# Optimization experiments

Measured on AMD Instinct MI355X. Metric: run time of the kernel, lower is better.

## Reference

```python
import jax, jax.numpy as jnp
import numpy as np

N_QUBITS = 8
N_LAYERS = 2
BATCH = 16384


def setup_inputs() -> dict:
    key = jax.random.key(0)
    k1, k2 = jax.random.split(key)
    inputs = jax.random.normal(k1, (BATCH, N_QUBITS), dtype=jnp.float32)
    theta = (jax.random.normal(k2, (N_LAYERS, N_QUBITS, 3), dtype=jnp.float32) * 0.1)
    return {"inputs": inputs, "theta": theta}


def _apply_1q(state, U, q):
    # state: [B, 2, 2, ..., 2] (n qubit axes, wire q -> axis q+1)
    # U: [2, 2] (shared) or [B, 2, 2] (per-sample)
    s = jnp.moveaxis(state, q + 1, -1)
    if U.ndim == 3:
        s = jnp.einsum('bij,b...j->b...i', U, s)
    else:
        s = jnp.einsum('ij,b...j->b...i', U, s)
    return jnp.moveaxis(s, -1, q + 1)


def _cnot(state, c, t):
    # flip target axis where control bit == 1
    s0 = jax.lax.index_in_dim(state, 0, axis=c + 1, keepdims=True)
    s1 = jax.lax.index_in_dim(state, 1, axis=c + 1, keepdims=True)
    s1 = jnp.flip(s1, axis=t + 1)
    return jnp.concatenate([s0, s1], axis=c + 1)


def _circuit(inputs, theta):
    n = N_QUBITS
    B = inputs.shape[0]
    x = jnp.clip(inputs, -1.0, 1.0)
    # |0...0> initial state, batched
    state = jnp.zeros((B, 2 ** n), dtype=jnp.complex64).at[:, 0].set(1.0)
    state = state.reshape((B,) + (2,) * n)

    # ---- angle encoding: RY(pi * x_i) on wire i (per-sample gates) ----
    half = 0.5 * jnp.pi * x  # [B, n]
    c, s = jnp.cos(half), jnp.sin(half)
    for q in range(n):
        U = jnp.stack([jnp.stack([c[:, q], -s[:, q]], -1),
                       jnp.stack([s[:, q], c[:, q]], -1)], -2).astype(jnp.complex64)
        state = _apply_1q(state, U, q)

    # ---- variational layers: Rot(phi,th,om) = RZ(om) RY(th) RZ(phi), then CNOT chain ----
    for layer in range(N_LAYERS):
        for q in range(n):
            phi, th, om = theta[layer, q, 0], theta[layer, q, 1], theta[layer, q, 2]
            ct, st = jnp.cos(0.5 * th), jnp.sin(0.5 * th)
            u00 = jnp.exp(-0.5j * (phi + om)) * ct
            u01 = -jnp.exp(0.5j * (phi - om)) * st
            u10 = jnp.exp(-0.5j * (phi - om)) * st
            u11 = jnp.exp(0.5j * (phi + om)) * ct
            U = jnp.stack([jnp.stack([u00, u01]), jnp.stack([u10, u11])]).astype(jnp.complex64)
            state = _apply_1q(state, U, q)
        for q in range(n - 1):
            state = _cnot(state, q, q + 1)

    # ---- <Z_q> for each wire: marginal prob over qubit q ----
    prob = jnp.real(state * jnp.conj(state))  # [B, 2,...,2]
    exps = []
    for q in range(n):
        axes = tuple(a for a in range(1, n + 1) if a != q + 1)
        m = prob.sum(axis=axes)  # [B, 2]
        exps.append(m[:, 0] - m[:, 1])
    return jnp.stack(exps, axis=-1).astype(jnp.float32)  # [B, n]


def reference(inputs, theta):
    return _circuit(inputs, theta)
```

## Files before the change

### kernel.cpp

```cpp
#include <hip/hip_runtime.h>

#define PI_HALF_F 1.57079632679489661923f

template<int CTRL>
__device__ __forceinline__ float dpp1(float v) {
    return __int_as_float(__builtin_amdgcn_update_dpp(
        0, __float_as_int(v), CTRL, 0xF, 0xF, true));
}
#define QP_XOR1   0xB1
#define QP_XOR2   0x4E
#define QP_XOR3   0x1B
#define ROW_ROR4  0x124
#define ROW_ROR8  0x128
#define ROW_MIR   0x140
#define ROW_HMIR  0x141

template<int MASK>
__device__ __forceinline__ float xorlane(float v) {
    if constexpr (MASK == 1)  return dpp1<QP_XOR1>(v);
    else if constexpr (MASK == 2)  return dpp1<QP_XOR2>(v);
    else if constexpr (MASK == 3)  return dpp1<QP_XOR3>(v);
    else if constexpr (MASK == 4)  return dpp1<QP_XOR3>(dpp1<ROW_HMIR>(v));
    else if constexpr (MASK == 6)  return dpp1<QP_XOR1>(dpp1<ROW_HMIR>(v));
    else if constexpr (MASK == 8)  return dpp1<ROW_ROR8>(v);
    else                   return dpp1<QP_XOR3>(dpp1<ROW_MIR>(v));
}

template<int MASK>
__device__ __forceinline__ void lane_gate(float (&re)[16], float (&im)[16],
                                          float car, float cai, float cbr, float cbi) {
#pragma unroll
    for (int r = 0; r < 16; ++r) {
        const float ar = re[r], ai = im[r];
        const float br = xorlane<MASK>(ar);
        const float bi = xorlane<MASK>(ai);
        re[r] = car * ar - cai * ai + cbr * br - cbi * bi;
        im[r] = car * ai + cai * ar + cbr * bi + cbi * br;
    }
}

template<int MASK, int FBITS>
__device__ __forceinline__ void reg_gate(float (&re)[16], float (&im)[16],
        float c0r, float c0i, float d0r, float d0i,
        float c1r, float c1i, float d1r, float d1i) {
    constexpr int MSB = (MASK & 8) ? 8 : (MASK & 4) ? 4 : (MASK & 2) ? 2 : 1;
#pragma unroll
    for (int r = 0; r < 16; ++r) {
        if (r & MSB) continue;
        const int p = r ^ MASK;
        const bool f = __builtin_popcount(r & FBITS) & 1;
        const float ar = re[r], ai = im[r], br = re[p], bi = im[p];
        const float sAr = f ? c1r : c0r, sAi = f ? c1i : c0i;
        const float tAr = f ? d1r : d0r, tAi = f ? d1i : d0i;
        const float sBr = f ? c0r : c1r, sBi = f ? c0i : c1i;
        const float tBr = f ? d0r : d1r, tBi = f ? d0i : d1i;
        re[r] = sAr * ar - sAi * ai + tAr * br - tAi * bi;
        im[r] = sAr * ai + sAi * ar + tAr * bi + tAi * br;
        re[p] = sBr * br - sBi * bi + tBr * ar - tBi * ai;
        im[p] = sBr * bi + sBi * br + tBr * ai + tBi * ar;
    }
}

__global__ __launch_bounds__(256) void quantum_kernel(
    const float* __restrict__ x,
    const float* __restrict__ theta,
    float* __restrict__ out,
    int B)
{
    __shared__ float g[16][8];
    const int t = threadIdx.x;
    if (t < 16) {
        const int layer = t >> 3, q = t & 7;
        const float phi = theta[(layer * 8 + q) * 3 + 0];
        const float th  = theta[(layer * 8 + q) * 3 + 1];
        const float om  = theta[(layer * 8 + q) * 3 + 2];
        const float ct = __cosf(0.5f * th), st = __sinf(0.5f * th);
        const float a = 0.5f * (phi + om), b = 0.5f * (phi - om);
        const float ca = __cosf(a), sa = __sinf(a);
        const float cb = __cosf(b), sb = __sinf(b);
        g[t][0] =  ct * ca;  g[t][1] = -ct * sa;
        g[t][2] = -st * cb;  g[t][3] = -st * sb;
        g[t][4] =  st * cb;  g[t][5] = -st * sb;
        g[t][6] =  ct * ca;  g[t][7] =  ct * sa;
    }
    __syncthreads();

    const int tid = blockIdx.x * 256 + t;
    const int sample = tid >> 4;
    if (sample >= B) return;
    const int sub = t & 15;

    const float4* xp = reinterpret_cast<const float4*>(x + sample * 8);
    const float4 xa = xp[0], xb = xp[1];
    float xs[8] = {xa.x, xa.y, xa.z, xa.w, xb.x, xb.y, xb.z, xb.w};
    float cq[8], sq[8];
#pragma unroll
    for (int q = 0; q < 8; ++q) {
        float v = fminf(fmaxf(xs[q], -1.0f), 1.0f) * PI_HALF_F;
        cq[q] = __cosf(v);
        sq[q] = __sinf(v);
    }
    const float fa0 = (sub & 8) ? sq[0] : cq[0];
    const float fa1 = (sub & 4) ? sq[1] : cq[1];
    const float fa2 = (sub & 2) ? sq[2] : cq[2];
    const float fa3 = (sub & 1) ? sq[3] : cq[3];
    const float plane = fa0 * fa1 * fa2 * fa3;

    float h45[4], h67[4];
#pragma unroll
    for (int k = 0; k < 4; ++k) {
        h45[k] = ((k & 2) ? sq[4] : cq[4]) * ((k & 1) ? sq[5] : cq[5]) * plane;
        h67[k] = ((k & 2) ? sq[6] : cq[6]) * ((k & 1) ? sq[7] : cq[7]);
    }
    float re[16], im[16];
#pragma unroll
    for (int r = 0; r < 16; ++r) { re[r] = h45[r >> 2] * h67[r & 3]; im[r] = 0.0f; }

#define LOADG(idx) \
    const float4 ga = *reinterpret_cast<const float4*>(&g[idx][0]); \
    const float4 gb = *reinterpret_cast<const float4*>(&g[idx][4]); \
    const float u00r = ga.x, u00i = ga.y, u01r = ga.z, u01i = ga.w; \
    const float u10r = gb.x, u10i = gb.y, u11r = gb.z, u11i = gb.w;

#define LANE_COEFFS(hi) \
    const float car = (hi) ? u11r : u00r, cai = (hi) ? u11i : u00i; \
    const float cbr = (hi) ? u10r : u01r, cbi = (hi) ? u10i : u01i;

    const bool s3 = (sub >> 3) & 1, s2 = (sub >> 2) & 1, s1 = (sub >> 1) & 1, s0 = sub & 1;
    const bool par4 = s3 ^ s2 ^ s1 ^ s0;

    { LOADG(0); LANE_COEFFS(s3); lane_gate<8>(re, im, car, cai, cbr, cbi); }
    { LOADG(1); LANE_COEFFS(s2); lane_gate<4>(re, im, car, cai, cbr, cbi); }
    { LOADG(2); LANE_COEFFS(s1); lane_gate<2>(re, im, car, cai, cbr, cbi); }
    { LOADG(3); LANE_COEFFS(s0); lane_gate<1>(re, im, car, cai, cbr, cbi); }
    { LOADG(4); reg_gate<8,8>(re, im, u00r,u00i, u01r,u01i, u11r,u11i, u10r,u10i); }
    { LOADG(5); reg_gate<4,4>(re, im, u00r,u00i, u01r,u01i, u11r,u11i, u10r,u10i); }
    { LOADG(6); reg_gate<2,2>(re, im, u00r,u00i, u01r,u01i, u11r,u11i, u10r,u10i); }
    { LOADG(7); reg_gate<1,1>(re, im, u00r,u00i, u01r,u01i, u11r,u11i, u10r,u10i); }

    { LOADG(8);  LANE_COEFFS(s3);            lane_gate<12>(re, im, car, cai, cbr, cbi); }
    { LOADG(9);  LANE_COEFFS(s3 ^ s2);       lane_gate<6>(re, im, car, cai, cbr, cbi); }
    { LOADG(10); LANE_COEFFS(s3 ^ s2 ^ s1);  lane_gate<3>(re, im, car, cai, cbr, cbi); }
    {
        LOADG(11); LANE_COEFFS(par4);
#pragma unroll
        for (int r = 0; r < 8; ++r) {
            const float a0r = re[r],     a0i = im[r];
            const float a1r = re[r + 8], a1i = im[r + 8];
            const float b0r = xorlane<1>(a1r);
            const float b0i = xorlane<1>(a1i);
            const float b1r = xorlane<1>(a0r);
            const float b1i = xorlane<1>(a0i);
            re[r]     = car * a0r - cai * a0i + cbr * b0r - cbi * b0i;
            im[r]     = car * a0i + cai * a0r + cbr * b0i + cbi * b0r;
            re[r + 8] = car * a1r - cai * a1i + cbr * b1r - cbi * b1i;
            im[r + 8] = car * a1i + cai * a1r + cbr * b1i + cbi * b1r;
        }
    }
#define REG2_COEFFS() \
    const float c0r = par4 ? u11r : u00r, c0i = par4 ? u11i : u00i; \
    const float d0r = par4 ? u10r : u01r, d0i = par4 ? u10i : u01i; \
    const float c1r = par4 ? u00r : u11r, c1i = par4 ? u00i : u11i; \
    const float d1r = par4 ? u01r : u10r, d1i = par4 ? u01i : u10i;
    { LOADG(12); REG2_COEFFS(); reg_gate<12,8>(re, im, c0r,c0i,d0r,d0i,c1r,c1i,d1r,d1i); }
    { LOADG(13); REG2_COEFFS(); reg_gate<6,12>(re, im, c0r,c0i,d0r,d0i,c1r,c1i,d1r,d1i); }
    { LOADG(14); REG2_COEFFS(); reg_gate<3,14>(re, im, c0r,c0i,d0r,d0i,c1r,c1i,d1r,d1i); }
    { LOADG(15); REG2_COEFFS(); reg_gate<1,15>(re, im, c0r,c0i,d0r,d0i,c1r,c1i,d1r,d1i); }

    float A = 0.f, B3 = 0.f, B2 = 0.f, B31 = 0.f, B20 = 0.f;
#pragma unroll
    for (int r = 0; r < 16; ++r) {
        const float P = re[r] * re[r] + im[r] * im[r];
        A   += P;
        B3  += (r & 8) ? -P : P;
        B2  += (r & 4) ? -P : P;
        B31 += ((((r >> 3) ^ (r >> 1)) & 1) ? -P : P);
        B20 += ((((r >> 2) ^ r) & 1) ? -P : P);
    }
    const bool sgnA = s3 ^ s1;
    const bool sgnB = s2 ^ s0;
    float z0 = s3   ? -A   : A;
    float z1 = s2   ? -A   : A;
    float z2 = sgnA ? -A   : A;
    float z3 = sgnB ? -A   : A;
    float z4 = sgnA ? -B3  : B3;
    float z5 = sgnB ? -B2  : B2;
    float z6 = sgnA ? -B31 : B31;
    float z7 = sgnB ? -B20 : B20;

#define RED(z) \
    z += dpp1<QP_XOR1>(z); z += dpp1<QP_XOR2>(z); \
    z += dpp1<ROW_ROR4>(z); z += dpp1<ROW_ROR8>(z);
    RED(z0) RED(z1) RED(z2) RED(z3) RED(z4) RED(z5) RED(z6) RED(z7)
#undef RED

    if (sub < 8) {
        float v = z0;
        v = (sub == 1) ? z1 : v;
        v = (sub == 2) ? z2 : v;
        v = (sub == 3) ? z3 : v;
        v = (sub == 4) ? z4 : v;
        v = (sub == 5) ? z5 : v;
        v = (sub == 6) ? z6 : v;
        v = (sub == 7) ? z7 : v;
        out[sample * 8 + sub] = v;
    }
}

extern "C" void kernel_launch(void* const* d_in, const int* in_sizes, int n_in,
                              void* d_out, int out_size, void* d_ws, size_t ws_size,
                              hipStream_t stream) {
    const float* x     = (const float*)d_in[0];
    const float* theta = (const float*)d_in[1];
    float* out = (float*)d_out;
    const int B = in_sizes[0] / 8;
    const int threads_total = B * 16;
    const int blocks = (threads_total + 255) / 256;
    hipLaunchKernelGGL(quantum_kernel, dim3(blocks), dim3(256), 0, stream,
                       x, theta, out, B);
}
```

Measured before the change: 73.57 us.

## Process two samples per 16-lane group and use ds_swizzle for wide lane exchanges

Each 16-lane group now simulates two samples at once, with the gate routines interleaving both state vectors so the independent chains can hide DPP and FMA latency. Launching half as many threads also amortises the shared-memory gate coefficient loads and the setup work. Lane exchanges with masks 4, 6, 8 and 12 now use one ds_swizzle instead of chained DPP ops. In exchange, register use roughly doubles, which may lower occupancy, and ds_swizzle goes through the LDS crossbar with higher latency than DPP. The kernel also assumes B is even.

```diff
diff --git a/kernel.cpp b/kernel.cpp
--- a/kernel.cpp
+++ b/kernel.cpp
@@ -12,35 +12,41 @@
 #define QP_XOR3   0x1B
 #define ROW_ROR4  0x124
 #define ROW_ROR8  0x128
-#define ROW_MIR   0x140
-#define ROW_HMIR  0x141
 
 template<int MASK>
-__device__ __forceinline__ float xorlane(float v) {
-    if constexpr (MASK == 1)  return dpp1<QP_XOR1>(v);
+__device__ __forceinline__ float swz(float v) {
+    return __int_as_float(__builtin_amdgcn_ds_swizzle(
+        __float_as_int(v), (MASK << 10) | 0x1F));
+}
+
+template<int MASK>
+__device__ __forceinline__ float XL(float v) {
+    if constexpr (MASK == 1)       return dpp1<QP_XOR1>(v);
     else if constexpr (MASK == 2)  return dpp1<QP_XOR2>(v);
     else if constexpr (MASK == 3)  return dpp1<QP_XOR3>(v);
-    else if constexpr (MASK == 4)  return dpp1<QP_XOR3>(dpp1<ROW_HMIR>(v));
-    else if constexpr (MASK == 6)  return dpp1<QP_XOR1>(dpp1<ROW_HMIR>(v));
-    else if constexpr (MASK == 8)  return dpp1<ROW_ROR8>(v);
-    else                   return dpp1<QP_XOR3>(dpp1<ROW_MIR>(v));
+    else                           return swz<MASK>(v);
 }
 
 template<int MASK>
-__device__ __forceinline__ void lane_gate(float (&re)[16], float (&im)[16],
-                                          float car, float cai, float cbr, float cbi) {
+__device__ __forceinline__ void lane_gate2(float (&reA)[16], float (&imA)[16],
+                                           float (&reB)[16], float (&imB)[16],
+                                           float car, float cai, float cbr, float cbi) {
 #pragma unroll
     for (int r = 0; r < 16; ++r) {
-        const float ar = re[r], ai = im[r];
-        const float br = xorlane<MASK>(ar);
-        const float bi = xorlane<MASK>(ai);
-        re[r] = car * ar - cai * ai + cbr * br - cbi * bi;
-        im[r] = car * ai + cai * ar + cbr * bi + cbi * br;
+        const float arA = reA[r], aiA = imA[r];
+        const float arB = reB[r], aiB = imB[r];
+        const float brA = XL<MASK>(arA), biA = XL<MASK>(aiA);
+        const float brB = XL<MASK>(arB), biB = XL<MASK>(aiB);
+        reA[r] = car * arA - cai * aiA + cbr * brA - cbi * biA;
+        imA[r] = car * aiA + cai * arA + cbr * biA + cbi * brA;
+        reB[r] = car * arB - cai * aiB + cbr * brB - cbi * biB;
+        imB[r] = car * aiB + cai * arB + cbr * biB + cbi * brB;
     }
 }
 
 template<int MASK, int FBITS>
-__device__ __forceinline__ void reg_gate(float (&re)[16], float (&im)[16],
+__device__ __forceinline__ void reg_gate2(float (&reA)[16], float (&imA)[16],
+        float (&reB)[16], float (&imB)[16],
         float c0r, float c0i, float d0r, float d0i,
         float c1r, float c1i, float d1r, float d1i) {
     constexpr int MSB = (MASK & 8) ? 8 : (MASK & 4) ? 4 : (MASK & 2) ? 2 : 1;
@@ -49,15 +55,24 @@
         if (r & MSB) continue;
         const int p = r ^ MASK;
         const bool f = __builtin_popcount(r & FBITS) & 1;
-        const float ar = re[r], ai = im[r], br = re[p], bi = im[p];
         const float sAr = f ? c1r : c0r, sAi = f ? c1i : c0i;
         const float tAr = f ? d1r : d0r, tAi = f ? d1i : d0i;
         const float sBr = f ? c0r : c1r, sBi = f ? c0i : c1i;
         const float tBr = f ? d0r : d1r, tBi = f ? d0i : d1i;
-        re[r] = sAr * ar - sAi * ai + tAr * br - tAi * bi;
-        im[r] = sAr * ai + sAi * ar + tAr * bi + tAi * br;
-        re[p] = sBr * br - sBi * bi + tBr * ar - tBi * ai;
-        im[p] = sBr * bi + sBi * br + tBr * ai + tBi * ar;
+        {
+            const float ar = reA[r], ai = imA[r], br = reA[p], bi = imA[p];
+            reA[r] = sAr * ar - sAi * ai + tAr * br - tAi * bi;
+            imA[r] = sAr * ai + sAi * ar + tAr * bi + tAi * br;
+            reA[p] = sBr * br - sBi * bi + tBr * ar - tBi * ai;
+            imA[p] = sBr * bi + sBi * br + tBr * ai + tBi * ar;
+        }
+        {
+            const float ar = reB[r], ai = imB[r], br = reB[p], bi = imB[p];
+            reB[r] = sAr * ar - sAi * ai + tAr * br - tAi * bi;
+            imB[r] = sAr * ai + sAi * ar + tAr * bi + tAi * br;
+            reB[p] = sBr * br - sBi * bi + tBr * ar - tBi * ai;
+            imB[p] = sBr * bi + sBi * br + tBr * ai + tBi * ar;
+        }
     }
 }
 
@@ -86,35 +101,44 @@
     __syncthreads();
 
     const int tid = blockIdx.x * 256 + t;
-    const int sample = tid >> 4;
-    if (sample >= B) return;
+    const int group = tid >> 4;
+    const int sA = group * 2;
+    if (sA >= B) return;
     const int sub = t & 15;
 
-    const float4* xp = reinterpret_cast<const float4*>(x + sample * 8);
-    const float4 xa = xp[0], xb = xp[1];
-    float xs[8] = {xa.x, xa.y, xa.z, xa.w, xb.x, xb.y, xb.z, xb.w};
-    float cq[8], sq[8];
-#pragma unroll
-    for (int q = 0; q < 8; ++q) {
-        float v = fminf(fmaxf(xs[q], -1.0f), 1.0f) * PI_HALF_F;
-        cq[q] = __cosf(v);
-        sq[q] = __sinf(v);
-    }
-    const float fa0 = (sub & 8) ? sq[0] : cq[0];
-    const float fa1 = (sub & 4) ? sq[1] : cq[1];
-    const float fa2 = (sub & 2) ? sq[2] : cq[2];
-    const float fa3 = (sub & 1) ? sq[3] : cq[3];
-    const float plane = fa0 * fa1 * fa2 * fa3;
-
-    float h45[4], h67[4];
-#pragma unroll
-    for (int k = 0; k < 4; ++k) {
-        h45[k] = ((k & 2) ? sq[4] : cq[4]) * ((k & 1) ? sq[5] : cq[5]) * plane;
-        h67[k] = ((k & 2) ? sq[6] : cq[6]) * ((k & 1) ? sq[7] : cq[7]);
-    }
-    float re[16], im[16];
-#pragma unroll
-    for (int r = 0; r < 16; ++r) { re[r] = h45[r >> 2] * h67[r & 3]; im[r] = 0.0f; }
+    const float4* xpA = reinterpret_cast<const float4*>(x + sA * 8);
+    const float4 xa0 = xpA[0], xa1 = xpA[1], xb0 = xpA[2], xb1 = xpA[3];
+    float xsA[8] = {xa0.x, xa0.y, xa0.z, xa0.w, xa1.x, xa1.y, xa1.z, xa1.w};
+    float xsB[8] = {xb0.x, xb0.y, xb0.z, xb0.w, xb1.x, xb1.y, xb1.z, xb1.w};
+
+    float reA[16], imA[16], reB[16], imB[16];
+    {
+        float cqA[8], sqA[8], cqB[8], sqB[8];
+#pragma unroll
+        for (int q = 0; q < 8; ++q) {
+            float vA = fminf(fmaxf(xsA[q], -1.0f), 1.0f) * PI_HALF_F;
+            float vB = fminf(fmaxf(xsB[q], -1.0f), 1.0f) * PI_HALF_F;
+            cqA[q] = __cosf(vA); sqA[q] = __sinf(vA);
+            cqB[q] = __cosf(vB); sqB[q] = __sinf(vB);
+        }
+        const float planeA = ((sub & 8) ? sqA[0] : cqA[0]) * ((sub & 4) ? sqA[1] : cqA[1])
+                           * ((sub & 2) ? sqA[2] : cqA[2]) * ((sub & 1) ? sqA[3] : cqA[3]);
+        const float planeB = ((sub & 8) ? sqB[0] : cqB[0]) * ((sub & 4) ? sqB[1] : cqB[1])
+                           * ((sub & 2) ? sqB[2] : cqB[2]) * ((sub & 1) ? sqB[3] : cqB[3]);
+        float h45A[4], h67A[4], h45B[4], h67B[4];
+#pragma unroll
+        for (int k = 0; k < 4; ++k) {
+            h45A[k] = ((k & 2) ? sqA[4] : cqA[4]) * ((k & 1) ? sqA[5] : cqA[5]) * planeA;
+            h67A[k] = ((k & 2) ? sqA[6] : cqA[6]) * ((k & 1) ? sqA[7] : cqA[7]);
+            h45B[k] = ((k & 2) ? sqB[4] : cqB[4]) * ((k & 1) ? sqB[5] : cqB[5]) * planeB;
+            h67B[k] = ((k & 2) ? sqB[6] : cqB[6]) * ((k & 1) ? sqB[7] : cqB[7]);
+        }
+#pragma unroll
+        for (int r = 0; r < 16; ++r) {
+            reA[r] = h45A[r >> 2] * h67A[r & 3]; imA[r] = 0.0f;
+            reB[r] = h45B[r >> 2] * h67B[r & 3]; imB[r] = 0.0f;
+        }
+    }
 
 #define LOADG(idx) \
     const float4 ga = *reinterpret_cast<const float4*>(&g[idx][0]); \
@@ -129,32 +153,42 @@
     const bool s3 = (sub >> 3) & 1, s2 = (sub >> 2) & 1, s1 = (sub >> 1) & 1, s0 = sub & 1;
     const bool par4 = s3 ^ s2 ^ s1 ^ s0;
 
-    { LOADG(0); LANE_COEFFS(s3); lane_gate<8>(re, im, car, cai, cbr, cbi); }
-    { LOADG(1); LANE_COEFFS(s2); lane_gate<4>(re, im, car, cai, cbr, cbi); }
-    { LOADG(2); LANE_COEFFS(s1); lane_gate<2>(re, im, car, cai, cbr, cbi); }
-    { LOADG(3); LANE_COEFFS(s0); lane_gate<1>(re, im, car, cai, cbr, cbi); }
-    { LOADG(4); reg_gate<8,8>(re, im, u00r,u00i, u01r,u01i, u11r,u11i, u10r,u10i); }
-    { LOADG(5); reg_gate<4,4>(re, im, u00r,u00i, u01r,u01i, u11r,u11i, u10r,u10i); }
-    { LOADG(6); reg_gate<2,2>(re, im, u00r,u00i, u01r,u01i, u11r,u11i, u10r,u10i); }
-    { LOADG(7); reg_gate<1,1>(re, im, u00r,u00i, u01r,u01i, u11r,u11i, u10r,u10i); }
-
-    { LOADG(8);  LANE_COEFFS(s3);            lane_gate<12>(re, im, car, cai, cbr, cbi); }
-    { LOADG(9);  LANE_COEFFS(s3 ^ s2);       lane_gate<6>(re, im, car, cai, cbr, cbi); }
-    { LOADG(10); LANE_COEFFS(s3 ^ s2 ^ s1);  lane_gate<3>(re, im, car, cai, cbr, cbi); }
+    { LOADG(0); LANE_COEFFS(s3); lane_gate2<8>(reA, imA, reB, imB, car, cai, cbr, cbi); }
+    { LOADG(1); LANE_COEFFS(s2); lane_gate2<4>(reA, imA, reB, imB, car, cai, cbr, cbi); }
+    { LOADG(2); LANE_COEFFS(s1); lane_gate2<2>(reA, imA, reB, imB, car, cai, cbr, cbi); }
+    { LOADG(3); LANE_COEFFS(s0); lane_gate2<1>(reA, imA, reB, imB, car, cai, cbr, cbi); }
+    { LOADG(4); reg_gate2<8,8>(reA, imA, reB, imB, u00r,u00i, u01r,u01i, u11r,u11i, u10r,u10i); }
+    { LOADG(5); reg_gate2<4,4>(reA, imA, reB, imB, u00r,u00i, u01r,u01i, u11r,u11i, u10r,u10i); }
+    { LOADG(6); reg_gate2<2,2>(reA, imA, reB, imB, u00r,u00i, u01r,u01i, u11r,u11i, u10r,u10i); }
+    { LOADG(7); reg_gate2<1,1>(reA, imA, reB, imB, u00r,u00i, u01r,u01i, u11r,u11i, u10r,u10i); }
+
+    { LOADG(8);  LANE_COEFFS(s3);           lane_gate2<12>(reA, imA, reB, imB, car, cai, cbr, cbi); }
+    { LOADG(9);  LANE_COEFFS(s3 ^ s2);      lane_gate2<6>(reA, imA, reB, imB, car, cai, cbr, cbi); }
+    { LOADG(10); LANE_COEFFS(s3 ^ s2 ^ s1); lane_gate2<3>(reA, imA, reB, imB, car, cai, cbr, cbi); }
     {
         LOADG(11); LANE_COEFFS(par4);
 #pragma unroll
         for (int r = 0; r < 8; ++r) {
-            const float a0r = re[r],     a0i = im[r];
-            const float a1r = re[r + 8], a1i = im[r + 8];
-            const float b0r = xorlane<1>(a1r);
-            const float b0i = xorlane<1>(a1i);
-            const float b1r = xorlane<1>(a0r);
-            const float b1i = xorlane<1>(a0i);
-            re[r]     = car * a0r - cai * a0i + cbr * b0r - cbi * b0i;
-            im[r]     = car * a0i + cai * a0r + cbr * b0i + cbi * b0r;
-            re[r + 8] = car * a1r - cai * a1i + cbr * b1r - cbi * b1i;
-            im[r + 8] = car * a1i + cai * a1r + cbr * b1i + cbi * b1r;
+            {
+                const float a0r = reA[r],     a0i = imA[r];
+                const float a1r = reA[r + 8], a1i = imA[r + 8];
+                const float b0r = dpp1<QP_XOR1>(a1r), b0i = dpp1<QP_XOR1>(a1i);
+                const float b1r = dpp1<QP_XOR1>(a0r), b1i = dpp1<QP_XOR1>(a0i);
+                reA[r]     = car * a0r - cai * a0i + cbr * b0r - cbi * b0i;
+                imA[r]     = car * a0i + cai * a0r + cbr * b0i + cbi * b0r;
+                reA[r + 8] = car * a1r - cai * a1i + cbr * b1r - cbi * b1i;
+                imA[r + 8] = car * a1i + cai * a1r + cbr * b1i + cbi * b1r;
+            }
+            {
+                const float a0r = reB[r],     a0i = imB[r];
+                const float a1r = reB[r + 8], a1i = imB[r + 8];
+                const float b0r = dpp1<QP_XOR1>(a1r), b0i = dpp1<QP_XOR1>(a1i);
+                const float b1r = dpp1<QP_XOR1>(a0r), b1i = dpp1<QP_XOR1>(a0i);
+                reB[r]     = car * a0r - cai * a0i + cbr * b0r - cbi * b0i;
+                imB[r]     = car * a0i + cai * a0r + cbr * b0i + cbi * b0r;
+                reB[r + 8] = car * a1r - cai * a1i + cbr * b1r - cbi * b1i;
+                imB[r + 8] = car * a1i + cai * a1r + cbr * b1i + cbi * b1r;
+            }
         }
     }
 #define REG2_COEFFS() \
@@ -162,49 +196,60 @@
     const float d0r = par4 ? u10r : u01r, d0i = par4 ? u10i : u01i; \
     const float c1r = par4 ? u00r : u11r, c1i = par4 ? u00i : u11i; \
     const float d1r = par4 ? u01r : u10r, d1i = par4 ? u01i : u10i;
-    { LOADG(12); REG2_COEFFS(); reg_gate<12,8>(re, im, c0r,c0i,d0r,d0i,c1r,c1i,d1r,d1i); }
-    { LOADG(13); REG2_COEFFS(); reg_gate<6,12>(re, im, c0r,c0i,d0r,d0i,c1r,c1i,d1r,d1i); }
-    { LOADG(14); REG2_COEFFS(); reg_gate<3,14>(re, im, c0r,c0i,d0r,d0i,c1r,c1i,d1r,d1i); }
-    { LOADG(15); REG2_COEFFS(); reg_gate<1,15>(re, im, c0r,c0i,d0r,d0i,c1r,c1i,d1r,d1i); }
-
-    float A = 0.f, B3 = 0.f, B2 = 0.f, B31 = 0.f, B20 = 0.f;
-#pragma unroll
-    for (int r = 0; r < 16; ++r) {
-        const float P = re[r] * re[r] + im[r] * im[r];
-        A   += P;
-        B3  += (r & 8) ? -P : P;
-        B2  += (r & 4) ? -P : P;
-        B31 += ((((r >> 3) ^ (r >> 1)) & 1) ? -P : P);
-        B20 += ((((r >> 2) ^ r) & 1) ? -P : P);
-    }
-    const bool sgnA = s3 ^ s1;
-    const bool sgnB = s2 ^ s0;
-    float z0 = s3   ? -A   : A;
-    float z1 = s2   ? -A   : A;
-    float z2 = sgnA ? -A   : A;
-    float z3 = sgnB ? -A   : A;
-    float z4 = sgnA ? -B3  : B3;
-    float z5 = sgnB ? -B2  : B2;
-    float z6 = sgnA ? -B31 : B31;
-    float z7 = sgnB ? -B20 : B20;
+    { LOADG(12); REG2_COEFFS(); reg_gate2<12,8>(reA, imA, reB, imB, c0r,c0i,d0r,d0i,c1r,c1i,d1r,d1i); }
+    { LOADG(13); REG2_COEFFS(); reg_gate2<6,12>(reA, imA, reB, imB, c0r,c0i,d0r,d0i,c1r,c1i,d1r,d1i); }
+    { LOADG(14); REG2_COEFFS(); reg_gate2<3,14>(reA, imA, reB, imB, c0r,c0i,d0r,d0i,c1r,c1i,d1r,d1i); }
+    { LOADG(15); REG2_COEFFS(); reg_gate2<1,15>(reA, imA, reB, imB, c0r,c0i,d0r,d0i,c1r,c1i,d1r,d1i); }
+
+    const bool sgnA_ = s3 ^ s1;
+    const bool sgnB_ = s2 ^ s0;
+
+#define MEASURE(re_, im_, z0,z1,z2,z3,z4,z5,z6,z7) \
+    float A_ = 0.f, B3_ = 0.f, B2_ = 0.f, B31_ = 0.f, B20_ = 0.f; \
+    _Pragma("unroll") \
+    for (int r = 0; r < 16; ++r) { \
+        const float P = re_[r] * re_[r] + im_[r] * im_[r]; \
+        A_   += P; \
+        B3_  += (r & 8) ? -P : P; \
+        B2_  += (r & 4) ? -P : P; \
+        B31_ += ((((r >> 3) ^ (r >> 1)) & 1) ? -P : P); \
+        B20_ += ((((r >> 2) ^ r) & 1) ? -P : P); \
+    } \
+    float z0 = s3    ? -A_   : A_; \
+    float z1 = s2    ? -A_   : A_; \
+    float z2 = sgnA_ ? -A_   : A_; \
+    float z3 = sgnB_ ? -A_   : A_; \
+    float z4 = sgnA_ ? -B3_  : B3_; \
+    float z5 = sgnB_ ? -B2_  : B2_; \
+    float z6 = sgnA_ ? -B31_ : B31_; \
+    float z7 = sgnB_ ? -B20_ : B20_;
 
 #define RED(z) \
     z += dpp1<QP_XOR1>(z); z += dpp1<QP_XOR2>(z); \
     z += dpp1<ROW_ROR4>(z); z += dpp1<ROW_ROR8>(z);
-    RED(z0) RED(z1) RED(z2) RED(z3) RED(z4) RED(z5) RED(z6) RED(z7)
-#undef RED
-
-    if (sub < 8) {
-        float v = z0;
-        v = (sub == 1) ? z1 : v;
-        v = (sub == 2) ? z2 : v;
-        v = (sub == 3) ? z3 : v;
-        v = (sub == 4) ? z4 : v;
-        v = (sub == 5) ? z5 : v;
-        v = (sub == 6) ? z6 : v;
-        v = (sub == 7) ? z7 : v;
-        out[sample * 8 + sub] = v;
-    }
+
+    float vA, vB;
+    {
+        MEASURE(reA, imA, zA0, zA1, zA2, zA3, zA4, zA5, zA6, zA7)
+        RED(zA0) RED(zA1) RED(zA2) RED(zA3) RED(zA4) RED(zA5) RED(zA6) RED(zA7)
+        const int i = sub & 7;
+        float v = zA0;
+        v = (i == 1) ? zA1 : v; v = (i == 2) ? zA2 : v; v = (i == 3) ? zA3 : v;
+        v = (i == 4) ? zA4 : v; v = (i == 5) ? zA5 : v; v = (i == 6) ? zA6 : v;
+        v = (i == 7) ? zA7 : v;
+        vA = v;
+    }
+    {
+        MEASURE(reB, imB, zB0, zB1, zB2, zB3, zB4, zB5, zB6, zB7)
+        RED(zB0) RED(zB1) RED(zB2) RED(zB3) RED(zB4) RED(zB5) RED(zB6) RED(zB7)
+        const int i = sub & 7;
+        float v = zB0;
+        v = (i == 1) ? zB1 : v; v = (i == 2) ? zB2 : v; v = (i == 3) ? zB3 : v;
+        v = (i == 4) ? zB4 : v; v = (i == 5) ? zB5 : v; v = (i == 6) ? zB6 : v;
+        v = (i == 7) ? zB7 : v;
+        vB = v;
+    }
+    out[group * 16 + sub] = (sub < 8) ? vA : vB;
 }
 
 extern "C" void kernel_launch(void* const* d_in, const int* in_sizes, int n_in,
@@ -214,7 +259,7 @@
     const float* theta = (const float*)d_in[1];
     float* out = (float*)d_out;
     const int B = in_sizes[0] / 8;
-    const int threads_total = B * 16;
+    const int threads_total = (B / 2) * 16;
     const int blocks = (threads_total + 255) / 256;
     hipLaunchKernelGGL(quantum_kernel, dim3(blocks), dim3(256), 0, stream,
                        x, theta, out, B);
```

Result: no change. 74.65 us (+1.5%).

## Spread each sample's state over 32 lanes with 8 amplitudes per lane

Applied to the files above, without the earlier changes.

Each sample is now handled by 32 lanes instead of 16, so each lane keeps 8 complex amplitudes in registers instead of 16. Gates on qubits 0-4 become cross-lane exchanges, implemented with ds_swizzle for the masks that DPP cannot express. The CNOT-permuted gates and the final Z-expectation reduction are re-derived for the 5-lane-bit layout, and the reduction gains an extra swizzle step. The aim is lower register pressure and higher occupancy (launch bounds now request 8 blocks per CU). The cost is twice the threads, more cross-lane traffic, and swizzles that go through the LDS path and are slower than DPP.

```diff
diff --git a/kernel.cpp b/kernel.cpp
--- a/kernel.cpp
+++ b/kernel.cpp
@@ -12,48 +12,48 @@
 #define QP_XOR3   0x1B
 #define ROW_ROR4  0x124
 #define ROW_ROR8  0x128
-#define ROW_MIR   0x140
-#define ROW_HMIR  0x141
 
 template<int MASK>
-__device__ __forceinline__ float xorlane(float v) {
-    if constexpr (MASK == 1)  return dpp1<QP_XOR1>(v);
+__device__ __forceinline__ float swz(float v) {
+    return __int_as_float(__builtin_amdgcn_ds_swizzle(
+        __float_as_int(v), (MASK << 10) | 0x1F));
+}
+
+template<int MASK>
+__device__ __forceinline__ float XL(float v) {
+    if constexpr (MASK == 1)       return dpp1<QP_XOR1>(v);
     else if constexpr (MASK == 2)  return dpp1<QP_XOR2>(v);
     else if constexpr (MASK == 3)  return dpp1<QP_XOR3>(v);
-    else if constexpr (MASK == 4)  return dpp1<QP_XOR3>(dpp1<ROW_HMIR>(v));
-    else if constexpr (MASK == 6)  return dpp1<QP_XOR1>(dpp1<ROW_HMIR>(v));
-    else if constexpr (MASK == 8)  return dpp1<ROW_ROR8>(v);
-    else                   return dpp1<QP_XOR3>(dpp1<ROW_MIR>(v));
+    else                           return swz<MASK>(v);
 }
 
 template<int MASK>
-__device__ __forceinline__ void lane_gate(float (&re)[16], float (&im)[16],
+__device__ __forceinline__ void lane_gate(float (&re)[8], float (&im)[8],
                                           float car, float cai, float cbr, float cbi) {
 #pragma unroll
-    for (int r = 0; r < 16; ++r) {
+    for (int r = 0; r < 8; ++r) {
         const float ar = re[r], ai = im[r];
-        const float br = xorlane<MASK>(ar);
-        const float bi = xorlane<MASK>(ai);
+        const float br = XL<MASK>(ar), bi = XL<MASK>(ai);
         re[r] = car * ar - cai * ai + cbr * br - cbi * bi;
         im[r] = car * ai + cai * ar + cbr * bi + cbi * br;
     }
 }
 
 template<int MASK, int FBITS>
-__device__ __forceinline__ void reg_gate(float (&re)[16], float (&im)[16],
+__device__ __forceinline__ void reg_gate(float (&re)[8], float (&im)[8],
         float c0r, float c0i, float d0r, float d0i,
         float c1r, float c1i, float d1r, float d1i) {
-    constexpr int MSB = (MASK & 8) ? 8 : (MASK & 4) ? 4 : (MASK & 2) ? 2 : 1;
-#pragma unroll
-    for (int r = 0; r < 16; ++r) {
+    constexpr int MSB = (MASK & 4) ? 4 : (MASK & 2) ? 2 : 1;
+#pragma unroll
+    for (int r = 0; r < 8; ++r) {
         if (r & MSB) continue;
         const int p = r ^ MASK;
         const bool f = __builtin_popcount(r & FBITS) & 1;
-        const float ar = re[r], ai = im[r], br = re[p], bi = im[p];
         const float sAr = f ? c1r : c0r, sAi = f ? c1i : c0i;
         const float tAr = f ? d1r : d0r, tAi = f ? d1i : d0i;
         const float sBr = f ? c0r : c1r, sBi = f ? c0i : c1i;
         const float tBr = f ? d0r : d1r, tBi = f ? d0i : d1i;
+        const float ar = re[r], ai = im[r], br = re[p], bi = im[p];
         re[r] = sAr * ar - sAi * ai + tAr * br - tAi * bi;
         im[r] = sAr * ai + sAi * ar + tAr * bi + tAi * br;
         re[p] = sBr * br - sBi * bi + tBr * ar - tBi * ai;
@@ -61,7 +61,7 @@
     }
 }
 
-__global__ __launch_bounds__(256) void quantum_kernel(
+__global__ __launch_bounds__(256, 8) void quantum_kernel(
     const float* __restrict__ x,
     const float* __restrict__ theta,
     float* __restrict__ out,
@@ -86,35 +86,40 @@
     __syncthreads();
 
     const int tid = blockIdx.x * 256 + t;
-    const int sample = tid >> 4;
+    const int sample = tid >> 5;
     if (sample >= B) return;
-    const int sub = t & 15;
-
-    const float4* xp = reinterpret_cast<const float4*>(x + sample * 8);
-    const float4 xa = xp[0], xb = xp[1];
-    float xs[8] = {xa.x, xa.y, xa.z, xa.w, xb.x, xb.y, xb.z, xb.w};
-    float cq[8], sq[8];
-#pragma unroll
-    for (int q = 0; q < 8; ++q) {
-        float v = fminf(fmaxf(xs[q], -1.0f), 1.0f) * PI_HALF_F;
-        cq[q] = __cosf(v);
-        sq[q] = __sinf(v);
-    }
-    const float fa0 = (sub & 8) ? sq[0] : cq[0];
-    const float fa1 = (sub & 4) ? sq[1] : cq[1];
-    const float fa2 = (sub & 2) ? sq[2] : cq[2];
-    const float fa3 = (sub & 1) ? sq[3] : cq[3];
-    const float plane = fa0 * fa1 * fa2 * fa3;
-
-    float h45[4], h67[4];
-#pragma unroll
-    for (int k = 0; k < 4; ++k) {
-        h45[k] = ((k & 2) ? sq[4] : cq[4]) * ((k & 1) ? sq[5] : cq[5]) * plane;
-        h67[k] = ((k & 2) ? sq[6] : cq[6]) * ((k & 1) ? sq[7] : cq[7]);
-    }
-    float re[16], im[16];
-#pragma unroll
-    for (int r = 0; r < 16; ++r) { re[r] = h45[r >> 2] * h67[r & 3]; im[r] = 0.0f; }
+    const int sub = t & 31;
+
+    const bool b4 = (sub >> 4) & 1, b3 = (sub >> 3) & 1, b2 = (sub >> 2) & 1;
+    const bool b1 = (sub >> 1) & 1, b0 = sub & 1;
+    const bool par5 = b4 ^ b3 ^ b2 ^ b1 ^ b0;
+
+    float re[8], im[8];
+    {
+        const float4* xp = reinterpret_cast<const float4*>(x + sample * 8);
+        const float4 xa = xp[0], xb = xp[1];
+        const float xs[8] = {xa.x, xa.y, xa.z, xa.w, xb.x, xb.y, xb.z, xb.w};
+        float cq[8], sq[8];
+#pragma unroll
+        for (int q = 0; q < 8; ++q) {
+            const float v = fminf(fmaxf(xs[q], -1.0f), 1.0f) * PI_HALF_F;
+            cq[q] = __cosf(v);
+            sq[q] = __sinf(v);
+        }
+        const float plane = (b4 ? sq[0] : cq[0]) * (b3 ? sq[1] : cq[1])
+                          * (b2 ? sq[2] : cq[2]) * (b1 ? sq[3] : cq[3])
+                          * (b0 ? sq[4] : cq[4]);
+        const float h5l = plane * cq[5], h5h = plane * sq[5];
+        float h67[4];
+#pragma unroll
+        for (int k = 0; k < 4; ++k)
+            h67[k] = ((k & 2) ? sq[6] : cq[6]) * ((k & 1) ? sq[7] : cq[7]);
+#pragma unroll
+        for (int r = 0; r < 8; ++r) {
+            re[r] = ((r & 4) ? h5h : h5l) * h67[r & 3];
+            im[r] = 0.0f;
+        }
+    }
 
 #define LOADG(idx) \
     const float4 ga = *reinterpret_cast<const float4*>(&g[idx][0]); \
@@ -126,71 +131,70 @@
     const float car = (hi) ? u11r : u00r, cai = (hi) ? u11i : u00i; \
     const float cbr = (hi) ? u10r : u01r, cbi = (hi) ? u10i : u01i;
 
-    const bool s3 = (sub >> 3) & 1, s2 = (sub >> 2) & 1, s1 = (sub >> 1) & 1, s0 = sub & 1;
-    const bool par4 = s3 ^ s2 ^ s1 ^ s0;
-
-    { LOADG(0); LANE_COEFFS(s3); lane_gate<8>(re, im, car, cai, cbr, cbi); }
-    { LOADG(1); LANE_COEFFS(s2); lane_gate<4>(re, im, car, cai, cbr, cbi); }
-    { LOADG(2); LANE_COEFFS(s1); lane_gate<2>(re, im, car, cai, cbr, cbi); }
-    { LOADG(3); LANE_COEFFS(s0); lane_gate<1>(re, im, car, cai, cbr, cbi); }
-    { LOADG(4); reg_gate<8,8>(re, im, u00r,u00i, u01r,u01i, u11r,u11i, u10r,u10i); }
+    { LOADG(0); LANE_COEFFS(b4); lane_gate<16>(re, im, car, cai, cbr, cbi); }
+    { LOADG(1); LANE_COEFFS(b3); lane_gate<8>(re, im, car, cai, cbr, cbi); }
+    { LOADG(2); LANE_COEFFS(b2); lane_gate<4>(re, im, car, cai, cbr, cbi); }
+    { LOADG(3); LANE_COEFFS(b1); lane_gate<2>(re, im, car, cai, cbr, cbi); }
+    { LOADG(4); LANE_COEFFS(b0); lane_gate<1>(re, im, car, cai, cbr, cbi); }
     { LOADG(5); reg_gate<4,4>(re, im, u00r,u00i, u01r,u01i, u11r,u11i, u10r,u10i); }
     { LOADG(6); reg_gate<2,2>(re, im, u00r,u00i, u01r,u01i, u11r,u11i, u10r,u10i); }
     { LOADG(7); reg_gate<1,1>(re, im, u00r,u00i, u01r,u01i, u11r,u11i, u10r,u10i); }
 
-    { LOADG(8);  LANE_COEFFS(s3);            lane_gate<12>(re, im, car, cai, cbr, cbi); }
-    { LOADG(9);  LANE_COEFFS(s3 ^ s2);       lane_gate<6>(re, im, car, cai, cbr, cbi); }
-    { LOADG(10); LANE_COEFFS(s3 ^ s2 ^ s1);  lane_gate<3>(re, im, car, cai, cbr, cbi); }
+    { LOADG(8);  LANE_COEFFS(b4);                lane_gate<24>(re, im, car, cai, cbr, cbi); }
+    { LOADG(9);  LANE_COEFFS(b4 ^ b3);           lane_gate<12>(re, im, car, cai, cbr, cbi); }
+    { LOADG(10); LANE_COEFFS(b4 ^ b3 ^ b2);      lane_gate<6>(re, im, car, cai, cbr, cbi); }
+    { LOADG(11); LANE_COEFFS(b4 ^ b3 ^ b2 ^ b1); lane_gate<3>(re, im, car, cai, cbr, cbi); }
     {
-        LOADG(11); LANE_COEFFS(par4);
-#pragma unroll
-        for (int r = 0; r < 8; ++r) {
+        LOADG(12); LANE_COEFFS(par5);
+#pragma unroll
+        for (int r = 0; r < 4; ++r) {
             const float a0r = re[r],     a0i = im[r];
-            const float a1r = re[r + 8], a1i = im[r + 8];
-            const float b0r = xorlane<1>(a1r);
-            const float b0i = xorlane<1>(a1i);
-            const float b1r = xorlane<1>(a0r);
-            const float b1i = xorlane<1>(a0i);
-            re[r]     = car * a0r - cai * a0i + cbr * b0r - cbi * b0i;
-            im[r]     = car * a0i + cai * a0r + cbr * b0i + cbi * b0r;
-            re[r + 8] = car * a1r - cai * a1i + cbr * b1r - cbi * b1i;
-            im[r + 8] = car * a1i + cai * a1r + cbr * b1i + cbi * b1r;
+            const float a1r = re[r + 4], a1i = im[r + 4];
+            const float p0r = dpp1<QP_XOR1>(a1r), p0i = dpp1<QP_XOR1>(a1i);
+            const float p1r = dpp1<QP_XOR1>(a0r), p1i = dpp1<QP_XOR1>(a0i);
+            re[r]     = car * a0r - cai * a0i + cbr * p0r - cbi * p0i;
+            im[r]     = car * a0i + cai * a0r + cbr * p0i + cbi * p0r;
+            re[r + 4] = car * a1r - cai * a1i + cbr * p1r - cbi * p1i;
+            im[r + 4] = car * a1i + cai * a1r + cbr * p1i + cbi * p1r;
         }
     }
 #define REG2_COEFFS() \
-    const float c0r = par4 ? u11r : u00r, c0i = par4 ? u11i : u00i; \
-    const float d0r = par4 ? u10r : u01r, d0i = par4 ? u10i : u01i; \
-    const float c1r = par4 ? u00r : u11r, c1i = par4 ? u00i : u11i; \
-    const float d1r = par4 ? u01r : u10r, d1i = par4 ? u01i : u10i;
-    { LOADG(12); REG2_COEFFS(); reg_gate<12,8>(re, im, c0r,c0i,d0r,d0i,c1r,c1i,d1r,d1i); }
-    { LOADG(13); REG2_COEFFS(); reg_gate<6,12>(re, im, c0r,c0i,d0r,d0i,c1r,c1i,d1r,d1i); }
-    { LOADG(14); REG2_COEFFS(); reg_gate<3,14>(re, im, c0r,c0i,d0r,d0i,c1r,c1i,d1r,d1i); }
-    { LOADG(15); REG2_COEFFS(); reg_gate<1,15>(re, im, c0r,c0i,d0r,d0i,c1r,c1i,d1r,d1i); }
-
-    float A = 0.f, B3 = 0.f, B2 = 0.f, B31 = 0.f, B20 = 0.f;
-#pragma unroll
-    for (int r = 0; r < 16; ++r) {
-        const float P = re[r] * re[r] + im[r] * im[r];
-        A   += P;
-        B3  += (r & 8) ? -P : P;
-        B2  += (r & 4) ? -P : P;
-        B31 += ((((r >> 3) ^ (r >> 1)) & 1) ? -P : P);
-        B20 += ((((r >> 2) ^ r) & 1) ? -P : P);
-    }
-    const bool sgnA = s3 ^ s1;
-    const bool sgnB = s2 ^ s0;
-    float z0 = s3   ? -A   : A;
-    float z1 = s2   ? -A   : A;
-    float z2 = sgnA ? -A   : A;
-    float z3 = sgnB ? -A   : A;
-    float z4 = sgnA ? -B3  : B3;
-    float z5 = sgnB ? -B2  : B2;
-    float z6 = sgnA ? -B31 : B31;
-    float z7 = sgnB ? -B20 : B20;
+    const float c0r = par5 ? u11r : u00r, c0i = par5 ? u11i : u00i; \
+    const float d0r = par5 ? u10r : u01r, d0i = par5 ? u10i : u01i; \
+    const float c1r = par5 ? u00r : u11r, c1i = par5 ? u00i : u11i; \
+    const float d1r = par5 ? u01r : u10r, d1i = par5 ? u01i : u10i;
+    { LOADG(13); REG2_COEFFS(); reg_gate<6,4>(re, im, c0r,c0i,d0r,d0i,c1r,c1i,d1r,d1i); }
+    { LOADG(14); REG2_COEFFS(); reg_gate<3,6>(re, im, c0r,c0i,d0r,d0i,c1r,c1i,d1r,d1i); }
+    { LOADG(15); REG2_COEFFS(); reg_gate<1,7>(re, im, c0r,c0i,d0r,d0i,c1r,c1i,d1r,d1i); }
+
+    float P[8];
+#pragma unroll
+    for (int r = 0; r < 8; ++r) P[r] = re[r] * re[r] + im[r] * im[r];
+
+    const float t01 = P[0] + P[1], t23 = P[2] + P[3];
+    const float t45 = P[4] + P[5], t67 = P[6] + P[7];
+    const float A  = (t01 + t23) + (t45 + t67);
+    const float B5 = (t01 + t23) - (t45 + t67);
+    const float B6 = (t01 - t23) + (t45 - t67);
+    const float B7 = (P[0] - P[1]) + (P[2] - P[3])
+                   - (P[4] - P[5]) - (P[6] - P[7]);
+
+    const bool gOdd  = b3 ^ b1;
+    const bool gEven = b4 ^ b2;
+    const bool gEv0  = gEven ^ b0;
+    float z0 = b4    ? -A  : A;
+    float z1 = b3    ? -A  : A;
+    float z2 = gEven ? -A  : A;
+    float z3 = gOdd  ? -A  : A;
+    float z4 = gEv0  ? -A  : A;
+    float z5 = gOdd  ? -B5 : B5;
+    float z6 = gEv0  ? -B6 : B6;
+    float z7 = gOdd  ? -B7 : B7;
 
 #define RED(z) \
     z += dpp1<QP_XOR1>(z); z += dpp1<QP_XOR2>(z); \
-    z += dpp1<ROW_ROR4>(z); z += dpp1<ROW_ROR8>(z);
+    z += dpp1<ROW_ROR4>(z); z += dpp1<ROW_ROR8>(z); \
+    z += swz<16>(z);
     RED(z0) RED(z1) RED(z2) RED(z3) RED(z4) RED(z5) RED(z6) RED(z7)
 #undef RED
 
@@ -214,8 +218,8 @@
     const float* theta = (const float*)d_in[1];
     float* out = (float*)d_out;
     const int B = in_sizes[0] / 8;
-    const int threads_total = B * 16;
-    const int blocks = (threads_total + 255) / 256;
+    const long long threads_total = (long long)B * 32;
+    const int blocks = (int)((threads_total + 255) / 256);
     hipLaunchKernelGGL(quantum_kernel, dim3(blocks), dim3(256), 0, stream,
                        x, theta, out, B);
 }
```

Result: faster. 70.33 us (-4.4%).
